# Kernel tuning notes

Hardware: AMD Instinct MI355X
Metric: run time of the kernel (lower is better)

The kernel has to match this reference:

```python
import jax, jax.numpy as jnp
import numpy as np

N_INST = 64  # number of distinct instance colors generated (color = 4*label, label 0 = background)
LAMBDA_SEP = 300.0


def setup_inputs() -> dict:
    key = jax.random.key(0)
    k1, k2 = jax.random.split(key)
    B, H, W = 4, 768, 768
    labels = jax.random.randint(k1, (B, H, W), 0, N_INST)
    labels = labels.at[:, :8, :8].set(0)  # guarantee background pixels exist (torch code assumes bg_pred is set)
    # target colors: (4*l, 4*l, 4*l) in [0, 252]; background label 0 -> (0,0,0)
    target = jnp.broadcast_to((labels * 4).astype(jnp.float32)[:, None, :, :], (B, 3, H, W))
    prediction = jax.random.uniform(k2, (B, 3, H, W), dtype=jnp.float32) * 255.0
    no_bg = jnp.zeros((B,), dtype=bool)
    return {"prediction": prediction, "target": target, "no_bg": no_bg}


def _huber(x, c):
    # elementwise huber, delta=1.0 (torch default)
    d = jnp.abs(x - c)
    return jnp.where(d < 1.0, 0.5 * d * d, d - 0.5)


def _per_image(P, L, nobg):
    # P: [N,3] predicted colors, L: [N] int instance labels (0 = background)
    N = P.shape[0]
    counts = jax.ops.segment_sum(jnp.ones((N,), P.dtype), L, num_segments=N_INST)  # [K]
    safe = jnp.maximum(counts, 1.0)
    means = jax.ops.segment_sum(P, L, num_segments=N_INST) / safe[:, None]  # [K,3]
    # intra-instance huber toward constant target (255 for instances, 0 for background), mean over 3*count elems
    h255 = _huber(P, 255.0).sum(-1)  # [N]
    h0 = _huber(P, 0.0).sum(-1)
    var = jax.ops.segment_sum(h255, L, num_segments=N_INST) / (3.0 * safe)
    var0 = jax.ops.segment_sum(h0, L, num_segments=N_INST) / (3.0 * safe)
    var = var.at[0].set(var0[0])
    # pixel -> instance-mean squared distances [N,K] (separation term)
    D = jnp.sum((P[:, None, :] - means[None, :, :]) ** 2, axis=-1)
    inv = LAMBDA_SEP / (1.0 + D)  # [N,K]
    bg_mask = (L == 0).astype(P.dtype)  # [N]
    bg_cnt = bg_mask.sum()
    nbg_cnt = jnp.asarray(N, P.dtype) - bg_cnt
    # non-bg instance k: mean over background pixels of 300/(1+||p - mean_k||^2)
    sep = (bg_mask @ inv) / jnp.maximum(bg_cnt, 1.0)  # [K]
    # background instance: mean over non-background pixels vs bg mean
    sep0 = ((1.0 - bg_mask) @ inv[:, 0]) / jnp.maximum(nbg_cnt, 1.0)
    sep = sep.at[0].set(sep0)
    w = 10.0 / jnp.sqrt(safe)
    present = counts > 0
    included = present.at[0].set(jnp.logical_and(present[0], jnp.logical_not(nobg)))
    incl = included.astype(P.dtype)
    ct = jnp.maximum(incl.sum(), 1.0)
    return jnp.sum(incl * (var + w * sep)) / ct


def reference(prediction, target, no_bg):
    B = prediction.shape[0]
    # recover integer instance labels from color map (generation: color = 4*label on all 3 channels)
    labels = jnp.round(target[:, 0] / 4.0).astype(jnp.int32).reshape(B, -1)  # [B,N]
    P = jnp.transpose(prediction, (0, 2, 3, 1)).reshape(B, -1, 3)  # [B,N,3]
    losses = jax.vmap(_per_image)(P, labels, no_bg)
    return jnp.mean(losses)
```

## Files before the change

### kernel.cpp

```cpp
#include <hip/hip_runtime.h>

#define NINST 64
#define ACC_STRIDE 512
#define OFF_CNT  0
#define OFF_SUM  64
#define OFF_H255 256
#define OFF_H0   320
#define LAMBDA_SEP 300.0f

#define P1_GX 288
#define P1_THREADS 256
#define P1_WAVES (P1_THREADS / 64)
#define P2_GX 128
#define P23_THREADS 1024
#define P3B 8
#define P3_TILE 1024
#define CNT_STRIDE 64
#define BGBUF 256

__device__ __forceinline__ float huber1(float x, float c) {
    float d = fabsf(x - c);
    return d < 1.0f ? 0.5f * d * d : d - 0.5f;
}

__global__ __launch_bounds__(P1_THREADS, 6)
void k_pass1(const float* __restrict__ pred, const float* __restrict__ targ,
             float* __restrict__ acc, unsigned* __restrict__ bgcnt,
             float* __restrict__ bglist, int maxbg, int N) {
    __shared__ float4 s_stage[P1_WAVES][256];
    __shared__ float4 s_red[P1_WAVES][NINST];
    __shared__ float s_corr255[NINST];
    __shared__ float s_corr0;
    __shared__ float s_bgbuf[BGBUF * 3];
    __shared__ unsigned s_bgn;
    __shared__ unsigned s_base;
    int tid = threadIdx.x;
    int lane = tid & 63;
    int wv = tid >> 6;
    int grp = lane >> 3;
    int s8 = (lane & 7) << 3;
    if (tid < NINST) s_corr255[tid] = 0.0f;
    if (tid == 0) { s_corr0 = 0.0f; s_bgn = 0u; }
    __syncthreads();

    int b = blockIdx.y;
    const float* bp = pred + (size_t)b * 3 * N;
    const float* bt = targ + (size_t)b * 3 * N;
    const float4* t0 = (const float4*)bt;
    const float4* p0 = (const float4*)bp;
    const float4* p1 = (const float4*)(bp + N);
    const float4* p2 = (const float4*)(bp + 2 * N);
    unsigned* bgc = &bgcnt[(size_t)b * CNT_STRIDE];
    float* bgl = bglist + (size_t)b * maxbg * 3;
    float* g = acc + (size_t)b * ACC_STRIDE;

    float cnt[8], sx[8], sy[8], sz[8];
#pragma unroll
    for (int t = 0; t < 8; t++) { cnt[t] = 0.0f; sx[t] = 0.0f; sy[t] = 0.0f; sz[t] = 0.0f; }

    int M = N >> 2;
    int stride = gridDim.x * blockDim.x;
    for (int base = blockIdx.x * blockDim.x + wv * 64; base < M; base += stride) {
        int i = base + lane;
        float xx[4], yy[4], zz[4];
        int labs[4];
        if (i < M) {
            float4 t = t0[i], a = p0[i], c = p1[i], d = p2[i];
            float tt[4] = {t.x, t.y, t.z, t.w};
            xx[0] = a.x; xx[1] = a.y; xx[2] = a.z; xx[3] = a.w;
            yy[0] = c.x; yy[1] = c.y; yy[2] = c.z; yy[3] = c.w;
            zz[0] = d.x; zz[1] = d.y; zz[2] = d.z; zz[3] = d.w;
#pragma unroll
            for (int j = 0; j < 4; j++) {
                int lab = (int)(tt[j] * 0.25f + 0.5f);
                labs[j] = lab;
                float dx = 255.0f - xx[j], dy = 255.0f - yy[j], dz = 255.0f - zz[j];
                float corr = 0.0f;
                if (dx < 1.0f) { float e = 1.0f - dx; corr += 0.5f * e * e; }
                if (dy < 1.0f) { float e = 1.0f - dy; corr += 0.5f * e * e; }
                if (dz < 1.0f) { float e = 1.0f - dz; corr += 0.5f * e * e; }
                if (corr != 0.0f) atomicAdd(&s_corr255[lab], corr);
                if (lab == 0) {
                    float c0 = 0.0f;
                    if (xx[j] < 1.0f) { float e = 1.0f - xx[j]; c0 += 0.5f * e * e; }
                    if (yy[j] < 1.0f) { float e = 1.0f - yy[j]; c0 += 0.5f * e * e; }
                    if (zz[j] < 1.0f) { float e = 1.0f - zz[j]; c0 += 0.5f * e * e; }
                    if (c0 != 0.0f) atomicAdd(&s_corr0, c0);
                    unsigned idx = atomicAdd(&s_bgn, 1u);
                    if (idx < BGBUF) {
                        s_bgbuf[idx * 3 + 0] = xx[j];
                        s_bgbuf[idx * 3 + 1] = yy[j];
                        s_bgbuf[idx * 3 + 2] = zz[j];
                    } else {
                        unsigned gi = atomicAdd(bgc, 1u);
                        if ((int)gi < maxbg) {
                            bgl[(size_t)gi * 3 + 0] = xx[j];
                            bgl[(size_t)gi * 3 + 1] = yy[j];
                            bgl[(size_t)gi * 3 + 2] = zz[j];
                        }
                    }
                }
            }
        } else {
#pragma unroll
            for (int j = 0; j < 4; j++) { xx[j] = yy[j] = zz[j] = 0.0f; labs[j] = -1; }
        }
#pragma unroll
        for (int j = 0; j < 4; j++)
            s_stage[wv][j * 64 + lane] =
                make_float4(xx[j], yy[j], zz[j], __int_as_float(labs[j]));
#pragma unroll 4
        for (int j = 0; j < 32; j++) {
            float4 v = s_stage[wv][(j << 3) + grp];
            int rel = __float_as_int(v.w) - s8;
#pragma unroll
            for (int t = 0; t < 8; t++) {
                float m = (rel == t) ? 1.0f : 0.0f;
                cnt[t] += m;
                sx[t] = fmaf(m, v.x, sx[t]);
                sy[t] = fmaf(m, v.y, sy[t]);
                sz[t] = fmaf(m, v.z, sz[t]);
            }
        }
    }

#pragma unroll
    for (int q = 0; q < 4; q++)
        s_stage[wv][q * 64 + lane] = make_float4(cnt[q], sx[q], sy[q], sz[q]);
    __syncthreads();
    if (lane < 32) {
        int s = lane & 7, q = lane >> 3;
        float4 ra = make_float4(0.0f, 0.0f, 0.0f, 0.0f);
#pragma unroll
        for (int gg = 0; gg < 8; gg++) {
            float4 p = s_stage[wv][q * 64 + (gg << 3) + s];
            ra.x += p.x; ra.y += p.y; ra.z += p.z; ra.w += p.w;
        }
        s_red[wv][(s << 3) + q] = ra;
    }
    __syncthreads();
#pragma unroll
    for (int q = 0; q < 4; q++)
        s_stage[wv][q * 64 + lane] = make_float4(cnt[q + 4], sx[q + 4], sy[q + 4], sz[q + 4]);
    __syncthreads();
    if (lane < 32) {
        int s = lane & 7, q = lane >> 3;
        float4 rb = make_float4(0.0f, 0.0f, 0.0f, 0.0f);
#pragma unroll
        for (int gg = 0; gg < 8; gg++) {
            float4 p = s_stage[wv][q * 64 + (gg << 3) + s];
            rb.x += p.x; rb.y += p.y; rb.z += p.z; rb.w += p.w;
        }
        s_red[wv][(s << 3) + q + 4] = rb;
    }
    __syncthreads();

    unsigned nloc = s_bgn < (unsigned)BGBUF ? s_bgn : (unsigned)BGBUF;
    if (tid == 0) s_base = atomicAdd(bgc, nloc);
    __syncthreads();
    {
        unsigned base3 = s_base * 3u;
        unsigned lim3 = (unsigned)maxbg * 3u;
        for (unsigned i = tid; i < nloc * 3u; i += blockDim.x) {
            if (base3 + i < lim3) bgl[base3 + i] = s_bgbuf[i];
        }
    }

    if (tid < NINST) {
        float c = 0.0f, x = 0.0f, y = 0.0f, z = 0.0f;
#pragma unroll
        for (int w = 0; w < P1_WAVES; w++) {
            float4 r = s_red[w][tid];
            c += r.x; x += r.y; y += r.z; z += r.w;
        }
        float s3 = x + y + z;
        atomicAdd(&g[OFF_CNT + tid], c);
        atomicAdd(&g[OFF_SUM + tid * 3 + 0], x);
        atomicAdd(&g[OFF_SUM + tid * 3 + 1], y);
        atomicAdd(&g[OFF_SUM + tid * 3 + 2], z);
        atomicAdd(&g[OFF_H255 + tid], 763.5f * c - s3 + s_corr255[tid]);
        if (tid == 0) atomicAdd(&g[OFF_H0], s3 - 1.5f * c + s_corr0);
    }

    if (blockIdx.x == 0 && tid < (N & 3)) {
        int i = (M << 2) + tid;
        float t = bt[i], x = bp[i], y = bp[N + i], z = bp[2 * N + i];
        int lab = (int)(t * 0.25f + 0.5f);
        atomicAdd(&g[OFF_CNT + lab], 1.0f);
        atomicAdd(&g[OFF_SUM + lab * 3 + 0], x);
        atomicAdd(&g[OFF_SUM + lab * 3 + 1], y);
        atomicAdd(&g[OFF_SUM + lab * 3 + 2], z);
        atomicAdd(&g[OFF_H255 + lab], huber1(x, 255.f) + huber1(y, 255.f) + huber1(z, 255.f));
        if (lab == 0) {
            atomicAdd(&g[OFF_H0], huber1(x, 0.f) + huber1(y, 0.f) + huber1(z, 0.f));
            unsigned gi = atomicAdd(bgc, 1u);
            if ((int)gi < maxbg) {
                bgl[(size_t)gi * 3 + 0] = x;
                bgl[(size_t)gi * 3 + 1] = y;
                bgl[(size_t)gi * 3 + 2] = z;
            }
        }
    }
}

__global__ void k_pass23(const float* __restrict__ pred, const float* __restrict__ targ,
                         const float* __restrict__ acc, const float* __restrict__ bglist,
                         const unsigned* __restrict__ bgcnt, float* __restrict__ p2part,
                         float* __restrict__ p3part, int maxbg, int N) {
    __shared__ float s_w[16];
    __shared__ float s_px[P3_TILE * 3];
    __shared__ float s_part[16][NINST];
    int tid = threadIdx.x;
    int b = blockIdx.y;
    const float* g = acc + (size_t)b * ACC_STRIDE;

    if (blockIdx.x < P2_GX) {
        float safe0 = fmaxf(g[OFF_CNT + 0], 1.0f);
        float m0x = g[OFF_SUM + 0] / safe0;
        float m0y = g[OFF_SUM + 1] / safe0;
        float m0z = g[OFF_SUM + 2] / safe0;

        const float* base_p = pred + (size_t)b * 3 * N;
        const float* base_t = targ + (size_t)b * 3 * N;
        const float4* p0 = (const float4*)(base_p);
        const float4* p1 = (const float4*)(base_p + N);
        const float4* p2 = (const float4*)(base_p + 2 * N);
        const float4* t0 = (const float4*)(base_t);

        float local = 0.0f;
        int M = N >> 2;
        for (int i = blockIdx.x * blockDim.x + tid; i < M; i += P2_GX * blockDim.x) {
            float4 t = t0[i], a = p0[i], c = p1[i], d = p2[i];
            float ts[4] = {t.x, t.y, t.z, t.w};
            float xs[4] = {a.x, a.y, a.z, a.w};
            float ys[4] = {c.x, c.y, c.z, c.w};
            float zs[4] = {d.x, d.y, d.z, d.w};
#pragma unroll
            for (int j = 0; j < 4; j++) {
                float dx = xs[j] - m0x, dy = ys[j] - m0y, dz = zs[j] - m0z;
                float D = dx * dx + dy * dy + dz * dz;
                float m = (ts[j] > 2.0f) ? LAMBDA_SEP : 0.0f;
                local = fmaf(m, __builtin_amdgcn_rcpf(1.0f + D), local);
            }
        }
        if (blockIdx.x == 0) {
            for (int i = (M << 2) + tid; i < N; i += blockDim.x) {
                float dx = base_p[i] - m0x, dy = base_p[N + i] - m0y, dz = base_p[2 * N + i] - m0z;
                float D = dx * dx + dy * dy + dz * dz;
                float m = (base_t[i] > 2.0f) ? LAMBDA_SEP : 0.0f;
                local = fmaf(m, __builtin_amdgcn_rcpf(1.0f + D), local);
            }
        }
#pragma unroll
        for (int o = 32; o > 0; o >>= 1) local += __shfl_down(local, o, 64);
        int wv = tid >> 6;
        if ((tid & 63) == 0) s_w[wv] = local;
        __syncthreads();
        if (tid == 0) {
            float s = 0.0f;
            for (int i = 0; i < (P23_THREADS >> 6); i++) s += s_w[i];
            p2part[(size_t)b * P2_GX + blockIdx.x] = s;
        }
    } else {
        int bx = blockIdx.x - P2_GX;
        int lane = tid & 63;
        int wv = tid >> 6;
        float safe = fmaxf(g[OFF_CNT + lane], 1.0f);
        float mx = g[OFF_SUM + lane * 3 + 0] / safe;
        float my = g[OFF_SUM + lane * 3 + 1] / safe;
        float mz = g[OFF_SUM + lane * 3 + 2] / safe;

        int nb = min((int)bgcnt[(size_t)b * CNT_STRIDE], maxbg);
        const float* bgl = bglist + (size_t)b * maxbg * 3;

        float lacc = 0.0f;
        int ntiles = (nb + P3_TILE - 1) / P3_TILE;
        for (int tile = bx; tile < ntiles; tile += P3B) {
            int base = tile * P3_TILE;
            int cnt = min(P3_TILE, nb - base);
            __syncthreads();
            for (int i = tid; i < cnt * 3; i += blockDim.x) s_px[i] = bgl[(size_t)base * 3 + i];
            __syncthreads();
            int lim = cnt - wv * 64;
            lim = lim < 0 ? 0 : (lim > 64 ? 64 : lim);
            const float* px = &s_px[wv * 64 * 3];
            for (int j = 0; j < lim; j++) {
                float x = px[j * 3 + 0];
                float y = px[j * 3 + 1];
                float z = px[j * 3 + 2];
                float dx = x - mx, dy = y - my, dz = z - mz;
                float D = dx * dx + dy * dy + dz * dz;
                lacc += LAMBDA_SEP * __builtin_amdgcn_rcpf(1.0f + D);
            }
        }
        s_part[wv][lane] = lacc;
        __syncthreads();
        if (tid < NINST) {
            float s = 0.0f;
#pragma unroll
            for (int w = 0; w < 16; w++) s += s_part[w][tid];
            p3part[((size_t)b * P3B + bx) * NINST + tid] = s;
        }
    }
}

__global__ void k_final(const float* __restrict__ acc, const float* __restrict__ p2part,
                        const float* __restrict__ p3part, const unsigned char* __restrict__ nobg,
                        float* __restrict__ out, int N, int B) {
    int tid = threadIdx.x;
    float total = 0.0f;
    for (int b = 0; b < B; b++) {
        const float* g = acc + (size_t)b * ACC_STRIDE;
        float c = g[OFF_CNT + tid];
        float c0 = g[OFF_CNT + 0];
        bool incl = (c > 0.0f);
        if (tid == 0 && nobg[b] != 0) incl = false;
        float safe = fmaxf(c, 1.0f);
        float var = (tid == 0 ? g[OFF_H0] : g[OFF_H255 + tid]) / (3.0f * safe);
        float s2 = p2part[(size_t)b * P2_GX + tid] + p2part[(size_t)b * P2_GX + NINST + tid];
#pragma unroll
        for (int o = 32; o > 0; o >>= 1) s2 += __shfl_down(s2, o, 64);
        float sepnum;
        if (tid == 0) {
            sepnum = s2;
        } else {
            float s = 0.0f;
#pragma unroll
            for (int j = 0; j < P3B; j++) s += p3part[((size_t)b * P3B + j) * NINST + tid];
            sepnum = s;
        }
        float denom = (tid == 0) ? fmaxf((float)N - c0, 1.0f) : fmaxf(c0, 1.0f);
        float sep = sepnum / denom;
        float w = 10.0f / sqrtf(safe);
        float term = incl ? (var + w * sep) : 0.0f;
        float cnt = incl ? 1.0f : 0.0f;
#pragma unroll
        for (int o = 32; o > 0; o >>= 1) {
            term += __shfl_down(term, o, 64);
            cnt += __shfl_down(cnt, o, 64);
        }
        if (tid == 0) total += term / fmaxf(cnt, 1.0f);
    }
    if (tid == 0) out[0] = total / (float)B;
}

extern "C" void kernel_launch(void* const* d_in, const int* in_sizes, int n_in,
                              void* d_out, int out_size, void* d_ws, size_t ws_size,
                              hipStream_t stream) {
    const float* pred = (const float*)d_in[0];
    const float* targ = (const float*)d_in[1];
    const unsigned char* nobg = (const unsigned char*)d_in[2];
    float* out = (float*)d_out;

    int B = in_sizes[2];
    int N = in_sizes[0] / (3 * B);

    float* acc = (float*)d_ws;
    size_t acc_bytes = (size_t)B * ACC_STRIDE * sizeof(float);
    unsigned* bgcnt = (unsigned*)((char*)d_ws + acc_bytes);
    size_t head = acc_bytes + 4096;
    float* p2part = (float*)((char*)d_ws + head);
    size_t p2_bytes = (size_t)B * P2_GX * sizeof(float);
    float* p3part = p2part + (size_t)B * P2_GX;
    size_t p3_bytes = (size_t)B * P3B * NINST * sizeof(float);
    size_t list_off = head + p2_bytes + p3_bytes;
    list_off = (list_off + 255) & ~(size_t)255;
    float* bglist = (float*)((char*)d_ws + list_off);

    int maxbg = 0;
    if (ws_size > list_off) {
        size_t cap = (ws_size - list_off) / ((size_t)B * 3 * sizeof(float));
        maxbg = (int)(cap < (size_t)131072 ? cap : (size_t)131072);
    }

    hipMemsetAsync(d_ws, 0, head, stream);

    dim3 g1(P1_GX, B);
    k_pass1<<<g1, dim3(P1_THREADS), 0, stream>>>(pred, targ, acc, bgcnt, bglist, maxbg, N);
    dim3 g23(P2_GX + P3B, B);
    k_pass23<<<g23, dim3(P23_THREADS), 0, stream>>>(pred, targ, acc, bglist, bgcnt,
                                                    p2part, p3part, maxbg, N);
    k_final<<<dim3(1), dim3(64), 0, stream>>>(acc, p2part, p3part, nobg, out, N, B);
}
```

Baseline: 83.98 us.

## Shrink pass1 LDS, add wave-level early-outs, drop shared background buffer

Pass 1 now stages half as many float4 values per wave (two halves of 128) and reduces the per-wave histogram in four rounds, with no block barriers in between. The shared background staging buffer is gone, so background pixels are appended straight to the global list with a global atomic each. Huber corrections near 255 and background handling are skipped by wave-uniform max/min checks. The aim is lower LDS use for higher occupancy and fewer barriers and branches, at the cost of more global atomics on background pixels.

After: 123.6 us. 47.1% more time.

```diff
diff --git a/kernel.cpp b/kernel.cpp
--- a/kernel.cpp
+++ b/kernel.cpp
@@ -16,7 +16,6 @@
 #define P3B 8
 #define P3_TILE 1024
 #define CNT_STRIDE 64
-#define BGBUF 256
 
 __device__ __forceinline__ float huber1(float x, float c) {
     float d = fabsf(x - c);
@@ -27,20 +26,17 @@
 void k_pass1(const float* __restrict__ pred, const float* __restrict__ targ,
              float* __restrict__ acc, unsigned* __restrict__ bgcnt,
              float* __restrict__ bglist, int maxbg, int N) {
-    __shared__ float4 s_stage[P1_WAVES][256];
+    __shared__ float4 s_stage[P1_WAVES][128];
     __shared__ float4 s_red[P1_WAVES][NINST];
     __shared__ float s_corr255[NINST];
     __shared__ float s_corr0;
-    __shared__ float s_bgbuf[BGBUF * 3];
-    __shared__ unsigned s_bgn;
-    __shared__ unsigned s_base;
     int tid = threadIdx.x;
     int lane = tid & 63;
     int wv = tid >> 6;
     int grp = lane >> 3;
     int s8 = (lane & 7) << 3;
     if (tid < NINST) s_corr255[tid] = 0.0f;
-    if (tid == 0) { s_corr0 = 0.0f; s_bgn = 0u; }
+    if (tid == 0) s_corr0 = 0.0f;
     __syncthreads();
 
     int b = blockIdx.y;
@@ -62,109 +58,98 @@
     int stride = gridDim.x * blockDim.x;
     for (int base = blockIdx.x * blockDim.x + wv * 64; base < M; base += stride) {
         int i = base + lane;
-        float xx[4], yy[4], zz[4];
+        float xx[4], yy[4], zz[4], tt[4];
         int labs[4];
         if (i < M) {
             float4 t = t0[i], a = p0[i], c = p1[i], d = p2[i];
-            float tt[4] = {t.x, t.y, t.z, t.w};
+            tt[0] = t.x; tt[1] = t.y; tt[2] = t.z; tt[3] = t.w;
             xx[0] = a.x; xx[1] = a.y; xx[2] = a.z; xx[3] = a.w;
             yy[0] = c.x; yy[1] = c.y; yy[2] = c.z; yy[3] = c.w;
             zz[0] = d.x; zz[1] = d.y; zz[2] = d.z; zz[3] = d.w;
 #pragma unroll
+            for (int j = 0; j < 4; j++) labs[j] = (int)(tt[j] * 0.25f + 0.5f);
+        } else {
+#pragma unroll
             for (int j = 0; j < 4; j++) {
-                int lab = (int)(tt[j] * 0.25f + 0.5f);
-                labs[j] = lab;
-                float dx = 255.0f - xx[j], dy = 255.0f - yy[j], dz = 255.0f - zz[j];
+                xx[j] = yy[j] = zz[j] = 128.0f; tt[j] = 8.0f; labs[j] = -1;
+            }
+        }
+
+        float m01 = fmaxf(fmaxf(xx[0], yy[0]), fmaxf(zz[0], xx[1]));
+        float m11 = fmaxf(fmaxf(yy[1], zz[1]), fmaxf(xx[2], yy[2]));
+        float m21 = fmaxf(fmaxf(zz[2], xx[3]), fmaxf(yy[3], zz[3]));
+        if (fmaxf(fmaxf(m01, m11), m21) > 254.0f) {
+#pragma unroll
+            for (int j = 0; j < 4; j++) {
                 float corr = 0.0f;
-                if (dx < 1.0f) { float e = 1.0f - dx; corr += 0.5f * e * e; }
-                if (dy < 1.0f) { float e = 1.0f - dy; corr += 0.5f * e * e; }
-                if (dz < 1.0f) { float e = 1.0f - dz; corr += 0.5f * e * e; }
-                if (corr != 0.0f) atomicAdd(&s_corr255[lab], corr);
-                if (lab == 0) {
+                float ex = xx[j] - 254.0f, ey = yy[j] - 254.0f, ez = zz[j] - 254.0f;
+                if (ex > 0.0f) corr += 0.5f * ex * ex;
+                if (ey > 0.0f) corr += 0.5f * ey * ey;
+                if (ez > 0.0f) corr += 0.5f * ez * ez;
+                if (corr != 0.0f) atomicAdd(&s_corr255[labs[j]], corr);
+            }
+        }
+        float tq = fminf(fminf(tt[0], tt[1]), fminf(tt[2], tt[3]));
+        if (tq < 2.0f) {
+#pragma unroll
+            for (int j = 0; j < 4; j++) {
+                if (tt[j] < 2.0f) {
                     float c0 = 0.0f;
                     if (xx[j] < 1.0f) { float e = 1.0f - xx[j]; c0 += 0.5f * e * e; }
                     if (yy[j] < 1.0f) { float e = 1.0f - yy[j]; c0 += 0.5f * e * e; }
                     if (zz[j] < 1.0f) { float e = 1.0f - zz[j]; c0 += 0.5f * e * e; }
                     if (c0 != 0.0f) atomicAdd(&s_corr0, c0);
-                    unsigned idx = atomicAdd(&s_bgn, 1u);
-                    if (idx < BGBUF) {
-                        s_bgbuf[idx * 3 + 0] = xx[j];
-                        s_bgbuf[idx * 3 + 1] = yy[j];
-                        s_bgbuf[idx * 3 + 2] = zz[j];
-                    } else {
-                        unsigned gi = atomicAdd(bgc, 1u);
-                        if ((int)gi < maxbg) {
-                            bgl[(size_t)gi * 3 + 0] = xx[j];
-                            bgl[(size_t)gi * 3 + 1] = yy[j];
-                            bgl[(size_t)gi * 3 + 2] = zz[j];
-                        }
+                    unsigned gi = atomicAdd(bgc, 1u);
+                    if ((int)gi < maxbg) {
+                        bgl[(size_t)gi * 3 + 0] = xx[j];
+                        bgl[(size_t)gi * 3 + 1] = yy[j];
+                        bgl[(size_t)gi * 3 + 2] = zz[j];
                     }
                 }
             }
-        } else {
-#pragma unroll
-            for (int j = 0; j < 4; j++) { xx[j] = yy[j] = zz[j] = 0.0f; labs[j] = -1; }
-        }
-#pragma unroll
-        for (int j = 0; j < 4; j++)
-            s_stage[wv][j * 64 + lane] =
-                make_float4(xx[j], yy[j], zz[j], __int_as_float(labs[j]));
+        }
+
+#pragma unroll
+        for (int h = 0; h < 2; h++) {
+            s_stage[wv][lane] =
+                make_float4(xx[2 * h], yy[2 * h], zz[2 * h], __int_as_float(labs[2 * h]));
+            s_stage[wv][64 + lane] =
+                make_float4(xx[2 * h + 1], yy[2 * h + 1], zz[2 * h + 1],
+                            __int_as_float(labs[2 * h + 1]));
 #pragma unroll 4
-        for (int j = 0; j < 32; j++) {
-            float4 v = s_stage[wv][(j << 3) + grp];
-            int rel = __float_as_int(v.w) - s8;
-#pragma unroll
-            for (int t = 0; t < 8; t++) {
-                float m = (rel == t) ? 1.0f : 0.0f;
-                cnt[t] += m;
-                sx[t] = fmaf(m, v.x, sx[t]);
-                sy[t] = fmaf(m, v.y, sy[t]);
-                sz[t] = fmaf(m, v.z, sz[t]);
-            }
-        }
-    }
-
-#pragma unroll
-    for (int q = 0; q < 4; q++)
-        s_stage[wv][q * 64 + lane] = make_float4(cnt[q], sx[q], sy[q], sz[q]);
+            for (int j = 0; j < 16; j++) {
+                float4 v = s_stage[wv][(j << 3) + grp];
+                int rel = __float_as_int(v.w) - s8;
+#pragma unroll
+                for (int t = 0; t < 8; t++) {
+                    float m = (rel == t) ? 1.0f : 0.0f;
+                    cnt[t] += m;
+                    sx[t] = fmaf(m, v.x, sx[t]);
+                    sy[t] = fmaf(m, v.y, sy[t]);
+                    sz[t] = fmaf(m, v.z, sz[t]);
+                }
+            }
+        }
+    }
+
+#pragma unroll
+    for (int r = 0; r < 4; r++) {
+        s_stage[wv][lane] =
+            make_float4(cnt[2 * r], sx[2 * r], sy[2 * r], sz[2 * r]);
+        s_stage[wv][64 + lane] =
+            make_float4(cnt[2 * r + 1], sx[2 * r + 1], sy[2 * r + 1], sz[2 * r + 1]);
+        if (lane < 16) {
+            int s = lane & 7, qp = lane >> 3;
+            float4 ra = make_float4(0.0f, 0.0f, 0.0f, 0.0f);
+#pragma unroll
+            for (int gg = 0; gg < 8; gg++) {
+                float4 p = s_stage[wv][qp * 64 + (gg << 3) + s];
+                ra.x += p.x; ra.y += p.y; ra.z += p.z; ra.w += p.w;
+            }
+            s_red[wv][(s << 3) + 2 * r + qp] = ra;
+        }
+    }
     __syncthreads();
-    if (lane < 32) {
-        int s = lane & 7, q = lane >> 3;
-        float4 ra = make_float4(0.0f, 0.0f, 0.0f, 0.0f);
-#pragma unroll
-        for (int gg = 0; gg < 8; gg++) {
-            float4 p = s_stage[wv][q * 64 + (gg << 3) + s];
-            ra.x += p.x; ra.y += p.y; ra.z += p.z; ra.w += p.w;
-        }
-        s_red[wv][(s << 3) + q] = ra;
-    }
-    __syncthreads();
-#pragma unroll
-    for (int q = 0; q < 4; q++)
-        s_stage[wv][q * 64 + lane] = make_float4(cnt[q + 4], sx[q + 4], sy[q + 4], sz[q + 4]);
-    __syncthreads();
-    if (lane < 32) {
-        int s = lane & 7, q = lane >> 3;
-        float4 rb = make_float4(0.0f, 0.0f, 0.0f, 0.0f);
-#pragma unroll
-        for (int gg = 0; gg < 8; gg++) {
-            float4 p = s_stage[wv][q * 64 + (gg << 3) + s];
-            rb.x += p.x; rb.y += p.y; rb.z += p.z; rb.w += p.w;
-        }
-        s_red[wv][(s << 3) + q + 4] = rb;
-    }
-    __syncthreads();
-
-    unsigned nloc = s_bgn < (unsigned)BGBUF ? s_bgn : (unsigned)BGBUF;
-    if (tid == 0) s_base = atomicAdd(bgc, nloc);
-    __syncthreads();
-    {
-        unsigned base3 = s_base * 3u;
-        unsigned lim3 = (unsigned)maxbg * 3u;
-        for (unsigned i = tid; i < nloc * 3u; i += blockDim.x) {
-            if (base3 + i < lim3) bgl[base3 + i] = s_bgbuf[i];
-        }
-    }
 
     if (tid < NINST) {
         float c = 0.0f, x = 0.0f, y = 0.0f, z = 0.0f;
```
